# Kernel tuning notes

Hardware: AMD Instinct MI355X
Metric: run time of the kernel (lower is better)

## Reference

```python
import jax, jax.numpy as jnp
import numpy as np

B, N, C = 8, 1024, 768
H = 12
D = C // H  # head_dim = 64
SCALE = D ** -0.5
EPS = 1e-5


def _layer_norm(x):
    # per-head LayerNorm over last dim, gamma=1, beta=0, biased variance
    mean = x.mean(-1, keepdims=True)
    var = ((x - mean) ** 2).mean(-1, keepdims=True)
    return (x - mean) / jnp.sqrt(var + EPS)


def setup_inputs() -> dict:
    key = jax.random.key(0)
    k1, k2, k3 = jax.random.split(key, 3)
    x = jax.random.normal(k1, (B, N, C), dtype=jnp.float32)
    qkv_weight = jax.random.normal(k2, (3 * C, C), dtype=jnp.float32) * (C ** -0.5)
    proj_weight = jax.random.normal(k3, (C, C), dtype=jnp.float32) * (C ** -0.5)
    return {"x": x, "qkv_weight": qkv_weight, "proj_weight": proj_weight}


def reference(x, qkv_weight, proj_weight):
    Bx, Nx, Cx = x.shape
    qkv = x @ qkv_weight.T                          # [B,N,3C]
    qkv = qkv.reshape(Bx, Nx, 3, H, D).transpose(2, 0, 3, 1, 4)  # [3,B,H,N,D]
    q, k, v = qkv[0], qkv[1], qkv[2]
    q = _layer_norm(q) * SCALE
    k = _layer_norm(k)
    attn = jnp.einsum('bhnd,bhmd->bhnm', q, k)      # [B,H,N,N]
    attn = jax.nn.softmax(attn, axis=-1)
    out = jnp.einsum('bhnm,bhmd->bhnd', attn, v)    # [B,H,N,D]
    out = out.transpose(0, 2, 1, 3).reshape(Bx, Nx, Cx)
    return out @ proj_weight.T
```

## Files before the change

### kernel.cpp

```cpp
#include <hip/hip_runtime.h>
#include <stdint.h>
#include <stddef.h>

#define HB 8
#define HN 1024
#define HC 768
#define HH 12
#define HD 64
#define ROWS (HB*HN)
#define BH (HB*HH)

using s16x4  = __attribute__((ext_vector_type(4))) short;
using bf16x8 = __attribute__((ext_vector_type(8))) short;
using f32x4  = __attribute__((ext_vector_type(4))) float;

__device__ __forceinline__ short f2bf(float f) {
  union { float f; uint32_t u; } c; c.f = f;
  uint32_t u = c.u;
  uint32_t r = (u + 0x7fffu + ((u >> 16) & 1u)) >> 16;
  return (short)r;
}
__device__ __forceinline__ float bf2f(short s) {
  union { uint32_t u; float f; } c; c.u = ((uint32_t)(uint16_t)s) << 16;
  return c.f;
}
__device__ __forceinline__ uint32_t pack_bf16_rne(float a, float b) {
  union { float f; uint32_t u; } ca, cb; ca.f = a; cb.f = b;
  uint32_t ra = ca.u + 0x7fffu + ((ca.u >> 16) & 1u);
  uint32_t rb = cb.u + 0x7fffu + ((cb.u >> 16) & 1u);
  return __builtin_amdgcn_perm(rb, ra, 0x07060302);
}
__device__ __forceinline__ float fast_exp2(float x) {
#if __has_builtin(__builtin_amdgcn_exp2f)
  return __builtin_amdgcn_exp2f(x);
#else
  return exp2f(x);
#endif
}
__device__ __forceinline__ f32x4 mfma16(bf16x8 a, bf16x8 b, f32x4 c) {
  return __builtin_amdgcn_mfma_f32_16x16x32_bf16(a, b, c, 0, 0, 0);
}
__device__ __forceinline__ void gll16(const void* g, void* l) {
  __builtin_amdgcn_global_load_lds((const __attribute__((address_space(1))) void*)g,
                                   (__attribute__((address_space(3))) void*)l,
                                   16, 0, 0);
}

__global__ void cvt3_kernel(const float* __restrict__ x,  short* __restrict__ xb,  int n0,
                            const float* __restrict__ wq, short* __restrict__ wqb, int n1,
                            const float* __restrict__ wp, short* __restrict__ wpb, int n2) {
  int i = blockIdx.x * 256 + threadIdx.x;
  const float* in; short* out;
  if (i < n0)            { in = x;  out = xb;  }
  else if (i < n0 + n1)  { i -= n0; in = wq; out = wqb; }
  else if (i < n0 + n1 + n2) { i -= n0 + n1; in = wp; out = wpb; }
  else return;
  float4 v = ((const float4*)in)[i];
  s16x4 o;
  o.x = f2bf(v.x); o.y = f2bf(v.y); o.z = f2bf(v.z); o.w = f2bf(v.w);
  ((s16x4*)out)[i] = o;
}

__device__ __forceinline__ void store_c(float* p, float v) { *p = v; }
__device__ __forceinline__ void store_c(short* p, float v) { *p = f2bf(v); }

template<int VM, bool STG, int SLOT>
__device__ __forceinline__ void qkv_ktile(
    int kt, short* sA, short* sB,
    const short* Ag, const short* Bg,
    int wr, int wc, int quad, int lc,
    int aoff0, int aoff1, int boff0,
    int cA0, int cA1, int cB0,
    f32x4 (&acc)[4][4])
{
  if constexpr (VM == 3) asm volatile("s_waitcnt vmcnt(3)" ::: "memory");
  else                   asm volatile("s_waitcnt vmcnt(0)" ::: "memory");
  __builtin_amdgcn_s_barrier();
  if constexpr (STG) {
    constexpr int DST = (SLOT + 2) % 3;
    const int kcol = (kt + 2) * 32;
    short* dA = sA + DST*8192;
    short* dB = sB + DST*4096;
    gll16(Ag + (size_t)(aoff0 + kcol), (void*)(dA + cA0*8));
    gll16(Ag + (size_t)(aoff1 + kcol), (void*)(dA + cA1*8));
    gll16(Bg + (size_t)(boff0 + kcol), (void*)(dB + cB0*8));
  }
  const short* sa = sA + SLOT*8192;
  const short* sb = sB + SLOT*4096;
  bf16x8 af[4], bfr[4];
#pragma unroll
  for (int mt = 0; mt < 4; ++mt) {
    const int rA = wr*64 + mt*16 + lc;
    af[mt] = *(const bf16x8*)(sa + rA*32 + (quad ^ ((rA >> 1) & 3))*8);
  }
#pragma unroll
  for (int nt = 0; nt < 4; ++nt) {
    const int rB = wc*64 + nt*16 + lc;
    bfr[nt] = *(const bf16x8*)(sb + rB*32 + (quad ^ ((rB >> 1) & 3))*8);
  }
  __builtin_amdgcn_s_setprio(1);
#pragma unroll
  for (int mt = 0; mt < 4; ++mt)
#pragma unroll
    for (int nt = 0; nt < 4; ++nt)
      acc[mt][nt] = mfma16(af[mt], bfr[nt], acc[mt][nt]);
  __builtin_amdgcn_s_setprio(0);
}

__global__ __launch_bounds__(512, 4) void gemm_qkv(const short* __restrict__ A,
                                                   const short* __restrict__ Bw,
                                                   short* __restrict__ Qb,
                                                   short* __restrict__ Kb,
                                                   short* __restrict__ vb) {
  __shared__ short As[3*256*32];
  __shared__ short Bs[3*128*32];
  const int wg = blockIdx.x;
  const int swz = (wg & 7)*72 + (wg >> 3);
  const int by = swz / 18, bx = swz % 18;
  const int m0 = by*256, n0 = bx*128;
  const int tid = threadIdx.x;
  const int lane = tid & 63, w = tid >> 6, quad = lane >> 4, lc = lane & 15;
  const int wr = w >> 1, wc = w & 1;
  const int cA0 = tid,        rA0 = cA0 >> 2, sbA0 = ((cA0 & 3) ^ ((rA0 >> 1) & 3))*8;
  const int cA1 = 512 + tid,  rA1 = cA1 >> 2, sbA1 = ((cA1 & 3) ^ ((rA1 >> 1) & 3))*8;
  const int cB0 = tid,        rB0 = cB0 >> 2, sbB0 = ((cB0 & 3) ^ ((rB0 >> 1) & 3))*8;
  const int aoff0 = rA0*HC + sbA0;
  const int aoff1 = rA1*HC + sbA1;
  const int boff0 = rB0*HC + sbB0;
  const short* Ag = A  + (size_t)m0*HC;
  const short* Bg = Bw + (size_t)n0*HC;
  f32x4 acc[4][4] = {};

#pragma unroll
  for (int pk = 0; pk < 2; ++pk) {
    gll16(Ag + (size_t)(aoff0 + pk*32), (void*)(As + pk*8192 + cA0*8));
    gll16(Ag + (size_t)(aoff1 + pk*32), (void*)(As + pk*8192 + cA1*8));
    gll16(Bg + (size_t)(boff0 + pk*32), (void*)(Bs + pk*4096 + cB0*8));
  }

#pragma unroll 1
  for (int kt = 0; kt < 21; kt += 3) {
    qkv_ktile<3,true,0>(kt,   As, Bs, Ag, Bg, wr, wc, quad, lc,
                        aoff0, aoff1, boff0, cA0, cA1, cB0, acc);
    qkv_ktile<3,true,1>(kt+1, As, Bs, Ag, Bg, wr, wc, quad, lc,
                        aoff0, aoff1, boff0, cA0, cA1, cB0, acc);
    qkv_ktile<3,true,2>(kt+2, As, Bs, Ag, Bg, wr, wc, quad, lc,
                        aoff0, aoff1, boff0, cA0, cA1, cB0, acc);
  }
  qkv_ktile<3,true ,0>(21, As, Bs, Ag, Bg, wr, wc, quad, lc,
                       aoff0, aoff1, boff0, cA0, cA1, cB0, acc);
  qkv_ktile<3,false,1>(22, As, Bs, Ag, Bg, wr, wc, quad, lc,
                       aoff0, aoff1, boff0, cA0, cA1, cB0, acc);
  qkv_ktile<0,false,2>(23, As, Bs, Ag, Bg, wr, wc, quad, lc,
                       aoff0, aoff1, boff0, cA0, cA1, cB0, acc);

  const int cg = n0 + wc*64;
  const int t = cg / HC;
  const int h = (cg % HC) / HD;
  if (t < 2) {
    short* outp = (t == 0) ? Qb : Kb;
    const float sc = (t == 0) ? 0.125f : 1.0f;
#pragma unroll
    for (int i = 0; i < 4; ++i)
#pragma unroll
      for (int r = 0; r < 4; ++r) {
        float s1 = (acc[i][0][r] + acc[i][1][r]) + (acc[i][2][r] + acc[i][3][r]);
        float s2 = acc[i][0][r]*acc[i][0][r];
        s2 = __builtin_fmaf(acc[i][1][r], acc[i][1][r], s2);
        s2 = __builtin_fmaf(acc[i][2][r], acc[i][2][r], s2);
        s2 = __builtin_fmaf(acc[i][3][r], acc[i][3][r], s2);
#pragma unroll
        for (int off = 1; off < 16; off <<= 1) {
          s1 += __shfl_xor(s1, off);
          s2 += __shfl_xor(s2, off);
        }
        const float mean = s1 * (1.0f/64.0f);
        const float var  = s2 * (1.0f/64.0f) - mean*mean;
        const float inv  = rsqrtf(var + 1e-5f) * sc;
        const int row = m0 + wr*64 + i*16 + quad*4 + r;
        const int b = row >> 10, n_in = row & 1023;
        short* rowp = outp + ((size_t)(b*HH + h)*HN + n_in)*HD;
#pragma unroll
        for (int nt = 0; nt < 4; ++nt)
          rowp[nt*16 + lc] = f2bf((acc[i][nt][r] - mean) * inv);
      }
  } else {
#pragma unroll
    for (int i = 0; i < 4; ++i)
#pragma unroll
      for (int nt = 0; nt < 4; ++nt)
#pragma unroll
        for (int r = 0; r < 4; ++r) {
          const int row = m0 + wr*64 + i*16 + quad*4 + r;
          const int col = h*HD + nt*16 + lc;
          vb[(size_t)row*HC + col] = f2bf(acc[i][nt][r]);
        }
  }
}

__global__ __launch_bounds__(256) void gemm_bt_f32(const short* __restrict__ A,
                                                   const short* __restrict__ Bw,
                                                   float* __restrict__ C,
                                                   int M, int N, int K) {
  __shared__ short As[128*64];
  __shared__ short Bs[128*64];
  const int m0 = blockIdx.y * 128, n0 = blockIdx.x * 128;
  const int tid = threadIdx.x;
  const int lane = tid & 63, w = tid >> 6, quad = lane >> 4, lc = lane & 15;
  const int wr = w >> 1, wc = w & 1;
  f32x4 acc[4][4] = {};
  for (int kt = 0; kt < K; kt += 64) {
#pragma unroll
    for (int i = 0; i < 4; ++i) {
      const int chunk = i*256 + tid;
      const int r = chunk >> 3, cb = chunk & 7;
      const int cbs = cb ^ (r & 7);
      gll16(A  + (size_t)(m0 + r)*K + kt + cbs*8, (void*)(As + (size_t)chunk*8));
      gll16(Bw + (size_t)(n0 + r)*K + kt + cbs*8, (void*)(Bs + (size_t)chunk*8));
    }
    __syncthreads();
#pragma unroll
    for (int kk = 0; kk < 2; ++kk) {
      bf16x8 af[4], bfr[4];
      const int kb = kk*4 + quad;
#pragma unroll
      for (int mt = 0; mt < 4; ++mt)
        af[mt] = *(const bf16x8*)(As + (wr*64 + mt*16 + lc)*64 + (kb ^ (lc & 7))*8);
#pragma unroll
      for (int nt = 0; nt < 4; ++nt)
        bfr[nt] = *(const bf16x8*)(Bs + (wc*64 + nt*16 + lc)*64 + (kb ^ (lc & 7))*8);
#pragma unroll
      for (int mt = 0; mt < 4; ++mt)
#pragma unroll
        for (int nt = 0; nt < 4; ++nt)
          acc[mt][nt] = mfma16(af[mt], bfr[nt], acc[mt][nt]);
    }
    __syncthreads();
  }
#pragma unroll
  for (int mt = 0; mt < 4; ++mt)
#pragma unroll
    for (int nt = 0; nt < 4; ++nt)
#pragma unroll
      for (int r = 0; r < 4; ++r) {
        const int row = m0 + wr*64 + mt*16 + quad*4 + r;
        const int col = n0 + wc*64 + nt*16 + lc;
        store_c(C + (size_t)row*N + col, acc[mt][nt][r]);
      }
}

__global__ __launch_bounds__(256) void vtrans_kernel(const short* __restrict__ vb,
                                                     short* __restrict__ Vtb) {
  const int blk = blockIdx.x;
  const int tile = blk & 7, bh = blk >> 3;
  const int b = bh / HH, h = bh % HH;
  const int n0 = tile * 128;
  const int tid = threadIdx.x;
  __shared__ float vt[128][65];
#pragma unroll
  for (int i = 0; i < 32; ++i) {
    const int idx = i*256 + tid; const int r = idx >> 6, dcol = idx & 63;
    vt[r][dcol] = bf2f(vb[(size_t)(b*HN + n0 + r)*HC + h*HD + dcol]);
  }
  __syncthreads();
#pragma unroll
  for (int it = 0; it < 4; ++it) {
    const int idx = it*256 + tid;
    const int dd = idx >> 4, j8 = idx & 15;
    bf16x8 o;
#pragma unroll
    for (int u = 0; u < 8; ++u) {
      const int c  = j8*8 + u;
      const int g  = c >> 6, cl = c & 63;
      const int k  = g*64 + ((cl & 3)*16 + (cl >> 2));
      o[u] = f2bf(vt[k][dd]);
    }
    *(bf16x8*)(Vtb + ((size_t)bh*HD + dd)*HN + n0 + j8*8) = o;
  }
}

__global__ __launch_bounds__(256, 3) void attn_kernel(const short* __restrict__ Qb,
                                                      const short* __restrict__ Kb,
                                                      const short* __restrict__ Vtb,
                                                      short* __restrict__ AOb) {
  const int blk = blockIdx.x;
  const int qt = blk & 7, bh = blk >> 3;
  const int b = bh / HH, h = bh % HH;
  const int tid = threadIdx.x, w = tid >> 6, lane = tid & 63;
  const int quad = lane >> 4, lc = lane & 15;

  __shared__ short Ks [64][72];
  __shared__ short Vts[64][72];
  __shared__ short Ps [4][32][72];

  bf16x8 aq[2][2];
#pragma unroll
  for (int mt = 0; mt < 2; ++mt) {
    const int mrow = qt*128 + w*32 + mt*16 + lc;
    aq[mt][0] = *(const bf16x8*)(Qb + ((size_t)bh*HN + mrow)*HD + quad*8);
    aq[mt][1] = *(const bf16x8*)(Qb + ((size_t)bh*HN + mrow)*HD + 32 + quad*8);
  }

  const short* kbh = Kb  + (size_t)bh*HN*HD;
  const short* vbh = Vtb + (size_t)bh*HD*HN;

  f32x4 oacc[2][4] = {};
  float l_i[2][4] = {};

  bf16x8 gk[2], gv[2];
#pragma unroll
  for (int i = 0; i < 2; ++i) {
    const int c = i*256 + tid;
    gk[i] = *(const bf16x8*)(kbh + (size_t)(c >> 3)*HD + (c & 7)*8);
    gv[i] = *(const bf16x8*)(vbh + (size_t)(c >> 3)*HN + (c & 7)*8);
  }
#pragma unroll
  for (int i = 0; i < 2; ++i) {
    const int c = i*256 + tid;
    *(bf16x8*)(&Ks [c >> 3][(c & 7)*8]) = gk[i];
    *(bf16x8*)(&Vts[c >> 3][(c & 7)*8]) = gv[i];
  }
  __syncthreads();

  const float LOG2E = 1.44269504f;
  const float MB2   = 8.0f * 1.44269504f;

  for (int ck = 0; ck < 16; ++ck) {
    if (ck < 15) {
      const int nn0 = (ck + 1)*64;
#pragma unroll
      for (int i = 0; i < 2; ++i) {
        const int c = i*256 + tid;
        gk[i] = *(const bf16x8*)(kbh + (size_t)(nn0 + (c >> 3))*HD + (c & 7)*8);
        gv[i] = *(const bf16x8*)(vbh + (size_t)(c >> 3)*HN + nn0 + (c & 7)*8);
      }
    }

    f32x4 sacc[2][4] = {};
#pragma unroll
    for (int kk = 0; kk < 2; ++kk)
#pragma unroll
      for (int nt = 0; nt < 4; ++nt) {
        bf16x8 bk = *(const bf16x8*)(&Ks[nt*16 + lc][kk*32 + quad*8]);
#pragma unroll
        for (int mt = 0; mt < 2; ++mt)
          sacc[mt][nt] = mfma16(aq[mt][kk], bk, sacc[mt][nt]);
      }

#pragma unroll
    for (int mt = 0; mt < 2; ++mt)
#pragma unroll
      for (int r = 0; r < 4; ++r) {
        float ps[4];
#pragma unroll
        for (int nt = 0; nt < 4; ++nt) {
          ps[nt] = fast_exp2(__builtin_fmaf(sacc[mt][nt][r], LOG2E, -MB2));
          sacc[mt][nt][r] = ps[nt];
        }
        l_i[mt][r] += (ps[0] + ps[1]) + (ps[2] + ps[3]);
        uint2 pk;
        pk.x = pack_bf16_rne(ps[0], ps[1]);
        pk.y = pack_bf16_rne(ps[2], ps[3]);
        *(uint2*)(&Ps[w][mt*16 + quad*4 + r][lc*4]) = pk;
      }

#pragma unroll
    for (int kk = 0; kk < 2; ++kk) {
      bf16x8 ap[2];
#pragma unroll
      for (int mt = 0; mt < 2; ++mt)
        ap[mt] = *(const bf16x8*)(&Ps[w][mt*16 + lc][kk*32 + quad*8]);
#pragma unroll
      for (int nt2 = 0; nt2 < 4; ++nt2) {
        bf16x8 bv = *(const bf16x8*)(&Vts[nt2*16 + lc][kk*32 + quad*8]);
#pragma unroll
        for (int mt = 0; mt < 2; ++mt)
          oacc[mt][nt2] = mfma16(ap[mt], bv, oacc[mt][nt2]);
      }
    }

    if (ck < 15) {
      __syncthreads();
#pragma unroll
      for (int i = 0; i < 2; ++i) {
        const int c = i*256 + tid;
        *(bf16x8*)(&Ks [c >> 3][(c & 7)*8]) = gk[i];
        *(bf16x8*)(&Vts[c >> 3][(c & 7)*8]) = gv[i];
      }
      __syncthreads();
    }
  }

#pragma unroll
  for (int mt = 0; mt < 2; ++mt)
#pragma unroll
    for (int r = 0; r < 4; ++r) {
      float l = l_i[mt][r];
#pragma unroll
      for (int off = 1; off < 16; off <<= 1) l += __shfl_xor(l, off);
      const float rl = 1.0f / l;
      const int row = qt*128 + w*32 + mt*16 + quad*4 + r;
#pragma unroll
      for (int nt2 = 0; nt2 < 4; ++nt2) {
        const int d = nt2*16 + lc;
        AOb[((size_t)(b*HN + row))*HC + h*HD + d] = f2bf(oacc[mt][nt2][r] * rl);
      }
    }
}

extern "C" void kernel_launch(void* const* d_in, const int* in_sizes, int n_in,
                              void* d_out, int out_size, void* d_ws, size_t ws_size,
                              hipStream_t stream) {
  const float* x     = (const float*)d_in[0];
  const float* wqkv  = (const float*)d_in[1];
  const float* wproj = (const float*)d_in[2];
  float* out = (float*)d_out;

  char* ws = (char*)d_ws;
  size_t off = 0;
  auto alloc = [&](size_t bytes) -> void* {
    void* p = ws + off; off += (bytes + 255) & ~(size_t)255; return p;
  };
  short* xb     = (short*)alloc((size_t)ROWS*HC*2);
  short* wqkvb  = (short*)alloc((size_t)3*HC*HC*2);
  short* wprojb = (short*)alloc((size_t)HC*HC*2);
  short* vb     = (short*)alloc((size_t)ROWS*HC*2);
  short* Qb     = (short*)alloc((size_t)BH*HN*HD*2);
  short* Kb     = (short*)alloc((size_t)BH*HN*HD*2);
  short* Vtb    = (short*)alloc((size_t)BH*HD*HN*2);
  short* AOb    = (short*)alloc((size_t)ROWS*HC*2);

  { const int n0 = ROWS*HC/4, n1 = 3*HC*HC/4, n2 = HC*HC/4;
    const int tot = n0 + n1 + n2;
    cvt3_kernel<<<(tot + 255)/256, 256, 0, stream>>>(x, xb, n0, wqkv, wqkvb, n1,
                                                     wproj, wprojb, n2); }

  gemm_qkv<<<dim3(576), 512, 0, stream>>>(xb, wqkvb, Qb, Kb, vb);
  vtrans_kernel<<<BH*8, 256, 0, stream>>>(vb, Vtb);
  attn_kernel<<<BH*8, 256, 0, stream>>>(Qb, Kb, Vtb, AOb);
  gemm_bt_f32<<<dim3(HC/128, ROWS/128), 256, 0, stream>>>(AOb, wprojb, out,
                                                          ROWS, HC, HC);
}
```

Before: 200.4 us.

## Fuse V transpose into QKV GEMM epilogue via shared-memory staging

The QKV GEMM epilogue for V tiles now stages results in shared memory in the permuted transposed order and writes Vt directly with vectorized stores. This removes the separate vtrans kernel launch and the intermediate vb buffer round trip through global memory. In exchange it adds two block syncs and LDS traffic to the V-tile blocks of the GEMM, and it reuses the GEMM's A/B shared buffers for staging.

New measurement: 185.1 us. -7.6%, faster.

```diff
diff --git a/kernel.cpp b/kernel.cpp
--- a/kernel.cpp
+++ b/kernel.cpp
@@ -111,9 +111,10 @@
                                                    const short* __restrict__ Bw,
                                                    short* __restrict__ Qb,
                                                    short* __restrict__ Kb,
-                                                   short* __restrict__ vb) {
-  __shared__ short As[3*256*32];
-  __shared__ short Bs[3*128*32];
+                                                   short* __restrict__ Vtb) {
+  __shared__ short SMEM[3*256*32 + 3*128*32];
+  short* As = SMEM;
+  short* Bs = SMEM + 3*256*32;
   const int wg = blockIdx.x;
   const int swz = (wg & 7)*72 + (wg >> 3);
   const int by = swz / 18, bx = swz % 18;
@@ -185,16 +186,37 @@
           rowp[nt*16 + lc] = f2bf((acc[i][nt][r] - mean) * inv);
       }
   } else {
+    short* vs = SMEM;
+    __syncthreads();
+    const int hd = wc;
 #pragma unroll
     for (int i = 0; i < 4; ++i)
 #pragma unroll
       for (int nt = 0; nt < 4; ++nt)
 #pragma unroll
         for (int r = 0; r < 4; ++r) {
-          const int row = m0 + wr*64 + i*16 + quad*4 + r;
-          const int col = h*HD + nt*16 + lc;
-          vb[(size_t)row*HC + col] = f2bf(acc[i][nt][r]);
+          const int dd = nt*16 + lc;
+          const int k  = i*16 + quad*4 + r;
+          const int c  = ((k & 15) << 2) | (k >> 4);
+          vs[(hd*64 + dd)*268 + wr*64 + c] = f2bf(acc[i][nt][r]);
         }
+    __syncthreads();
+    const int b = m0 >> 10, m0g = m0 & 1023;
+#pragma unroll
+    for (int it = 0; it < 8; ++it) {
+      const int idx = it*512 + tid;
+      const int h2 = idx >> 11;
+      const int rem = idx & 2047;
+      const int dd = rem >> 5, c8 = rem & 31;
+      const int habs = ((n0 + h2*64) - 1536) >> 6;
+      const short* src = vs + (h2*64 + dd)*268 + c8*8;
+      s16x4 lo = *(const s16x4*)(src);
+      s16x4 hi = *(const s16x4*)(src + 4);
+      bf16x8 vvv;
+      vvv[0]=lo[0]; vvv[1]=lo[1]; vvv[2]=lo[2]; vvv[3]=lo[3];
+      vvv[4]=hi[0]; vvv[5]=hi[1]; vvv[6]=hi[2]; vvv[7]=hi[3];
+      *(bf16x8*)(Vtb + ((size_t)((b*HH + habs)*HD + dd))*HN + m0g + c8*8) = vvv;
+    }
   }
 }
 
@@ -249,36 +271,6 @@
       }
 }
 
-__global__ __launch_bounds__(256) void vtrans_kernel(const short* __restrict__ vb,
-                                                     short* __restrict__ Vtb) {
-  const int blk = blockIdx.x;
-  const int tile = blk & 7, bh = blk >> 3;
-  const int b = bh / HH, h = bh % HH;
-  const int n0 = tile * 128;
-  const int tid = threadIdx.x;
-  __shared__ float vt[128][65];
-#pragma unroll
-  for (int i = 0; i < 32; ++i) {
-    const int idx = i*256 + tid; const int r = idx >> 6, dcol = idx & 63;
-    vt[r][dcol] = bf2f(vb[(size_t)(b*HN + n0 + r)*HC + h*HD + dcol]);
-  }
-  __syncthreads();
-#pragma unroll
-  for (int it = 0; it < 4; ++it) {
-    const int idx = it*256 + tid;
-    const int dd = idx >> 4, j8 = idx & 15;
-    bf16x8 o;
-#pragma unroll
-    for (int u = 0; u < 8; ++u) {
-      const int c  = j8*8 + u;
-      const int g  = c >> 6, cl = c & 63;
-      const int k  = g*64 + ((cl & 3)*16 + (cl >> 2));
-      o[u] = f2bf(vt[k][dd]);
-    }
-    *(bf16x8*)(Vtb + ((size_t)bh*HD + dd)*HN + n0 + j8*8) = o;
-  }
-}
-
 __global__ __launch_bounds__(256, 3) void attn_kernel(const short* __restrict__ Qb,
                                                       const short* __restrict__ Kb,
                                                       const short* __restrict__ Vtb,
@@ -424,7 +416,6 @@
   short* xb     = (short*)alloc((size_t)ROWS*HC*2);
   short* wqkvb  = (short*)alloc((size_t)3*HC*HC*2);
   short* wprojb = (short*)alloc((size_t)HC*HC*2);
-  short* vb     = (short*)alloc((size_t)ROWS*HC*2);
   short* Qb     = (short*)alloc((size_t)BH*HN*HD*2);
   short* Kb     = (short*)alloc((size_t)BH*HN*HD*2);
   short* Vtb    = (short*)alloc((size_t)BH*HD*HN*2);
@@ -435,8 +426,7 @@
     cvt3_kernel<<<(tot + 255)/256, 256, 0, stream>>>(x, xb, n0, wqkv, wqkvb, n1,
                                                      wproj, wprojb, n2); }
 
-  gemm_qkv<<<dim3(576), 512, 0, stream>>>(xb, wqkvb, Qb, Kb, vb);
-  vtrans_kernel<<<BH*8, 256, 0, stream>>>(vb, Vtb);
+  gemm_qkv<<<dim3(576), 512, 0, stream>>>(xb, wqkvb, Qb, Kb, Vtb);
   attn_kernel<<<BH*8, 256, 0, stream>>>(Qb, Kb, Vtb, AOb);
   gemm_bt_f32<<<dim3(HC/128, ROWS/128), 256, 0, stream>>>(AOb, wprojb, out,
                                                           ROWS, HC, HC);
```
